# Kernel optimization log

Hardware: AMD Instinct MI355X
Metric: run time of the kernel (lower is better)

Reference implementation:

```python
import jax, jax.numpy as jnp
import numpy as np


def setup_inputs() -> dict:
    key = jax.random.key(0)
    k1, k2, k3, k4 = jax.random.split(key, 4)
    N, E, DI, DO = 8192, 262144, 128, 128
    x = jax.random.normal(k1, (N, DI), dtype=jnp.float32)
    edge_index = jax.random.randint(k2, (2, E), 0, N, dtype=jnp.int64)
    W = jax.random.normal(k3, (DO, DI), dtype=jnp.float32) * (1.0 / np.sqrt(DI))
    b_lin = jax.random.normal(k4, (DO,), dtype=jnp.float32) * 0.01
    bias = jnp.zeros((DO,), dtype=jnp.float32)
    return {"x": x, "edge_index": edge_index, "W": W, "b_lin": b_lin, "bias": bias}


def reference(x, edge_index, W, b_lin, bias):
    # Linear: x @ W^T + b_lin  -> [N, DO]
    h = x @ W.T + b_lin
    N = h.shape[0]
    row, col = edge_index[0], edge_index[1]
    # Dense symmetric adjacency with 1.0 at (row,col) and (col,row); duplicates collapse (set, not add)
    adj = jnp.zeros((N, N), dtype=h.dtype)
    adj = adj.at[row, col].set(1.0)
    adj = adj.at[col, row].set(1.0)
    degree = jnp.sum(adj, axis=1)                      # [N]
    d_inv_sqrt = jnp.power(degree + 1e-6, -0.5)        # [N]
    # D^-1/2 A D^-1/2 as row/col scaling (same math as diag matmuls)
    normalized_adj = d_inv_sqrt[:, None] * adj * d_inv_sqrt[None, :]
    return normalized_adj @ h + bias
```

## Files before the change

kernel.cpp:

```cpp
#include <hip/hip_runtime.h>
#include <hip/hip_bf16.h>


#define DIM 128
#define ROWS_PER_BLOCK 16
#define MAXN 1024

__global__ __launch_bounds__(256) void setup_kernel(
    const float* __restrict__ x, const float* __restrict__ W,
    const float* __restrict__ b, __hip_bfloat16* __restrict__ hb,
    uint4* __restrict__ zero16, int nLin) {
    const int tid = threadIdx.x;
    if ((int)blockIdx.x >= nLin) {
        const long long idx = (long long)((int)blockIdx.x - nLin) * 256 + tid;
        zero16[idx] = make_uint4(0u, 0u, 0u, 0u);
        return;
    }
    __shared__ float xt[ROWS_PER_BLOCK * DIM];
    const int block_row = blockIdx.x * ROWS_PER_BLOCK;
    const float4* xg = reinterpret_cast<const float4*>(x + (long long)block_row * DIM);
    float4* xl = reinterpret_cast<float4*>(xt);
    for (int i = tid; i < ROWS_PER_BLOCK * (DIM / 4); i += 256) xl[i] = xg[i];
    __syncthreads();

    const int d = tid & 127;
    const int half = tid >> 7;
    const float4* W4 = reinterpret_cast<const float4*>(W + (long long)d * DIM);

    float acc[8] = {0.f, 0.f, 0.f, 0.f, 0.f, 0.f, 0.f, 0.f};
    for (int k4 = 0; k4 < DIM / 4; ++k4) {
        const float4 w = W4[k4];
#pragma unroll
        for (int j = 0; j < 8; ++j) {
            const float4 xv =
                reinterpret_cast<const float4*>(xt + (half * 8 + j) * DIM)[k4];
            acc[j] += w.x * xv.x + w.y * xv.y + w.z * xv.z + w.w * xv.w;
        }
    }
    const float bb = b[d];
#pragma unroll
    for (int j = 0; j < 8; ++j) {
        hb[(long long)(block_row + half * 8 + j) * DIM + d] =
            __float2bfloat16(acc[j] + bb);
    }
}

__global__ __launch_bounds__(256) void edge_kernel(
    const int* __restrict__ erow, const int* __restrict__ ecol,
    unsigned int* __restrict__ bitmap, int E, int WPR) {
    const int e = blockIdx.x * 256 + threadIdx.x;
    if (e >= E) return;
    const int r = erow[e];
    const int c = ecol[e];
    atomicOr(bitmap + (long long)r * WPR + (c >> 5), 1u << (c & 31));
    atomicOr(bitmap + (long long)c * WPR + (r >> 5), 1u << (r & 31));
}

__global__ __launch_bounds__(256) void degree_kernel(
    const unsigned int* __restrict__ bitmap, float* __restrict__ dinv, int WPR) {
    const int i = blockIdx.x * 4 + (threadIdx.x >> 6);
    const int lane = threadIdx.x & 63;
    const uint4* rowp = reinterpret_cast<const uint4*>(bitmap + (long long)i * WPR);
    const uint4 v = rowp[lane];
    int cnt = __popc(v.x) + __popc(v.y) + __popc(v.z) + __popc(v.w);
#pragma unroll
    for (int off = 32; off > 0; off >>= 1) cnt += __shfl_down(cnt, off);
    if (lane == 0) dinv[i] = rsqrtf((float)cnt + 1e-6f);
}

__global__ __launch_bounds__(256) void aggregate_kernel(
    const unsigned int* __restrict__ bitmap, const uint4* __restrict__ h16,
    const float* __restrict__ dinv, const float* __restrict__ bias,
    float* __restrict__ out, int WPR) {
    __shared__ int nbr[MAXN];
    __shared__ float wgt[MAXN];
    __shared__ int wave_sums[4];
    __shared__ float partial[16 * DIM];

    const int i = blockIdx.x;
    const int tid = threadIdx.x;
    const float d_i = dinv[i];
    const unsigned int* rowp = bitmap + (long long)i * WPR;

    unsigned int w = (tid < WPR) ? rowp[tid] : 0u;
    const int cnt = __popc(w);

    const int lane = tid & 63;
    const int wave = tid >> 6;
    int scan = cnt;
#pragma unroll
    for (int off = 1; off < 64; off <<= 1) {
        const int v = __shfl_up(scan, off);
        if (lane >= off) scan += v;
    }
    if (lane == 63) wave_sums[wave] = scan;
    __syncthreads();
    int wave_off = 0;
    for (int k = 0; k < wave; ++k) wave_off += wave_sums[k];
    int base = wave_off + scan - cnt;

    while (w) {
        const int bpos = __ffs(w) - 1;
        w &= w - 1;
        const int j = tid * 32 + bpos;
        if (base < MAXN) {
            nbr[base] = j;
            wgt[base] = dinv[j];
        }
        ++base;
    }
    __syncthreads();
    int cnt_total = wave_sums[0] + wave_sums[1] + wave_sums[2] + wave_sums[3];
    if (cnt_total > MAXN) cnt_total = MAXN;

    const int lane16 = tid & 15;
    const int g = tid >> 4;
    float a0 = 0.f, a1 = 0.f, a2 = 0.f, a3 = 0.f;
    float a4 = 0.f, a5 = 0.f, a6 = 0.f, a7 = 0.f;

#define ACC8(v, wv)                                                      \
    {                                                                    \
        a0 += (wv)*__uint_as_float((v).x << 16);                         \
        a1 += (wv)*__uint_as_float((v).x & 0xffff0000u);                 \
        a2 += (wv)*__uint_as_float((v).y << 16);                         \
        a3 += (wv)*__uint_as_float((v).y & 0xffff0000u);                 \
        a4 += (wv)*__uint_as_float((v).z << 16);                         \
        a5 += (wv)*__uint_as_float((v).z & 0xffff0000u);                 \
        a6 += (wv)*__uint_as_float((v).w << 16);                         \
        a7 += (wv)*__uint_as_float((v).w & 0xffff0000u);                 \
    }

    int m = g;
    for (; m + 48 < cnt_total; m += 64) {
        const int j0 = nbr[m], j1 = nbr[m + 16], j2 = nbr[m + 32], j3 = nbr[m + 48];
        const float w0 = wgt[m], w1 = wgt[m + 16], w2 = wgt[m + 32], w3 = wgt[m + 48];
        const uint4 v0 = h16[(j0 << 4) + lane16];
        const uint4 v1 = h16[(j1 << 4) + lane16];
        const uint4 v2 = h16[(j2 << 4) + lane16];
        const uint4 v3 = h16[(j3 << 4) + lane16];
        ACC8(v0, w0);
        ACC8(v1, w1);
        ACC8(v2, w2);
        ACC8(v3, w3);
    }
    for (; m < cnt_total; m += 16) {
        const int j = nbr[m];
        const float wm = wgt[m];
        const uint4 v = h16[(j << 4) + lane16];
        ACC8(v, wm);
    }
#undef ACC8

    float* p = partial + g * DIM + lane16 * 8;
    p[0] = a0; p[1] = a1; p[2] = a2; p[3] = a3;
    p[4] = a4; p[5] = a5; p[6] = a6; p[7] = a7;
    __syncthreads();

    if (tid < DIM) {
        float s = 0.f;
#pragma unroll
        for (int k = 0; k < 16; ++k) s += partial[k * DIM + tid];
        out[(long long)i * DIM + tid] = s * d_i + bias[tid];
    }
}

extern "C" void kernel_launch(void* const* d_in, const int* in_sizes, int n_in,
                              void* d_out, int out_size, void* d_ws, size_t ws_size,
                              hipStream_t stream) {
    const float* x = (const float*)d_in[0];
    const int* ei = (const int*)d_in[1];
    const float* W = (const float*)d_in[2];
    const float* b_lin = (const float*)d_in[3];
    const float* bias = (const float*)d_in[4];
    float* out = (float*)d_out;

    const int N = in_sizes[0] / DIM;
    const int E = in_sizes[1] / 2;
    const int WPR = (N + 31) >> 5;

    unsigned int* bitmap = (unsigned int*)d_ws;
    const long long bitmap_bytes = (long long)N * WPR * 4;
    float* dinv = (float*)((char*)d_ws + bitmap_bytes);
    __hip_bfloat16* hb =
        (__hip_bfloat16*)((char*)d_ws + bitmap_bytes + (long long)N * 4);

    const int nLin = N / ROWS_PER_BLOCK;
    const int nZero = (int)(bitmap_bytes / (256 * 16));
    setup_kernel<<<nLin + nZero, 256, 0, stream>>>(x, W, b_lin, hb,
                                                   (uint4*)bitmap, nLin);
    edge_kernel<<<(E + 255) / 256, 256, 0, stream>>>(ei, ei + E, bitmap, E, WPR);
    degree_kernel<<<N / 4, 256, 0, stream>>>(bitmap, dinv, WPR);
    aggregate_kernel<<<N, 256, 0, stream>>>(bitmap, (const uint4*)hb, dinv, bias,
                                            out, WPR);
}
```

Measured before the change: 63.44 us.

## Prescale features by inverse degree and regroup kernels to overlap edge scatter with linear

Zeroing the bitmap moves to its own kernel with nontemporal stores. The edge atomics and the linear layer now run as one launch on disjoint block ranges, so they can overlap. The degree kernel also multiplies each row of the bf16 h by its own d^-1/2, so the aggregate loop no longer gathers per-neighbor weights or does multiplies. In exchange h is rounded to bf16 a second time after scaling, and the degree kernel does an extra read and write of h.

```diff
diff --git a/kernel.cpp b/kernel.cpp
--- a/kernel.cpp
+++ b/kernel.cpp
@@ -6,18 +6,43 @@
 #define ROWS_PER_BLOCK 16
 #define MAXN 1024
 
-__global__ __launch_bounds__(256) void setup_kernel(
+typedef unsigned int u32x4 __attribute__((ext_vector_type(4)));
+
+__device__ inline unsigned short bf16bits(float f) {
+    __hip_bfloat16 b = __float2bfloat16(f);
+    return *reinterpret_cast<unsigned short*>(&b);
+}
+
+__device__ inline unsigned int scale2(unsigned int p, float s) {
+    const float lo = __uint_as_float(p << 16) * s;
+    const float hi = __uint_as_float(p & 0xffff0000u) * s;
+    return (unsigned int)bf16bits(lo) | ((unsigned int)bf16bits(hi) << 16);
+}
+
+__global__ __launch_bounds__(256) void zero_kernel(u32x4* __restrict__ p) {
+    const int idx = blockIdx.x * 256 + threadIdx.x;
+    u32x4 z = 0;
+    __builtin_nontemporal_store(z, p + idx);
+}
+
+__global__ __launch_bounds__(256) void edge_linear_kernel(
+    const int* __restrict__ erow, const int* __restrict__ ecol,
+    unsigned int* __restrict__ bitmap, int E, int WPR, int nEdge,
     const float* __restrict__ x, const float* __restrict__ W,
-    const float* __restrict__ b, __hip_bfloat16* __restrict__ hb,
-    uint4* __restrict__ zero16, int nLin) {
+    const float* __restrict__ b, __hip_bfloat16* __restrict__ hb) {
     const int tid = threadIdx.x;
-    if ((int)blockIdx.x >= nLin) {
-        const long long idx = (long long)((int)blockIdx.x - nLin) * 256 + tid;
-        zero16[idx] = make_uint4(0u, 0u, 0u, 0u);
+    if ((int)blockIdx.x < nEdge) {
+        const int e = blockIdx.x * 256 + tid;
+        if (e < E) {
+            const int r = erow[e];
+            const int c = ecol[e];
+            atomicOr(bitmap + (long long)r * WPR + (c >> 5), 1u << (c & 31));
+            atomicOr(bitmap + (long long)c * WPR + (r >> 5), 1u << (r & 31));
+        }
         return;
     }
     __shared__ float xt[ROWS_PER_BLOCK * DIM];
-    const int block_row = blockIdx.x * ROWS_PER_BLOCK;
+    const int block_row = ((int)blockIdx.x - nEdge) * ROWS_PER_BLOCK;
     const float4* xg = reinterpret_cast<const float4*>(x + (long long)block_row * DIM);
     float4* xl = reinterpret_cast<float4*>(xt);
     for (int i = tid; i < ROWS_PER_BLOCK * (DIM / 4); i += 256) xl[i] = xg[i];
@@ -45,27 +70,26 @@
     }
 }
 
-__global__ __launch_bounds__(256) void edge_kernel(
-    const int* __restrict__ erow, const int* __restrict__ ecol,
-    unsigned int* __restrict__ bitmap, int E, int WPR) {
-    const int e = blockIdx.x * 256 + threadIdx.x;
-    if (e >= E) return;
-    const int r = erow[e];
-    const int c = ecol[e];
-    atomicOr(bitmap + (long long)r * WPR + (c >> 5), 1u << (c & 31));
-    atomicOr(bitmap + (long long)c * WPR + (r >> 5), 1u << (r & 31));
-}
-
-__global__ __launch_bounds__(256) void degree_kernel(
-    const unsigned int* __restrict__ bitmap, float* __restrict__ dinv, int WPR) {
+__global__ __launch_bounds__(256) void degree_scale_kernel(
+    const unsigned int* __restrict__ bitmap, uint4* __restrict__ h16,
+    float* __restrict__ dinv, int WPR) {
     const int i = blockIdx.x * 4 + (threadIdx.x >> 6);
     const int lane = threadIdx.x & 63;
-    const uint4* rowp = reinterpret_cast<const uint4*>(bitmap + (long long)i * WPR);
-    const uint4 v = rowp[lane];
+    const uint4 v =
+        reinterpret_cast<const uint4*>(bitmap + (long long)i * WPR)[lane];
     int cnt = __popc(v.x) + __popc(v.y) + __popc(v.z) + __popc(v.w);
 #pragma unroll
-    for (int off = 32; off > 0; off >>= 1) cnt += __shfl_down(cnt, off);
-    if (lane == 0) dinv[i] = rsqrtf((float)cnt + 1e-6f);
+    for (int off = 1; off < 64; off <<= 1) cnt += __shfl_xor(cnt, off);
+    const float di = rsqrtf((float)cnt + 1e-6f);
+    if (lane == 0) dinv[i] = di;
+    if (lane < 16) {
+        uint4 hv = h16[i * 16 + lane];
+        hv.x = scale2(hv.x, di);
+        hv.y = scale2(hv.y, di);
+        hv.z = scale2(hv.z, di);
+        hv.w = scale2(hv.w, di);
+        h16[i * 16 + lane] = hv;
+    }
 }
 
 __global__ __launch_bounds__(256) void aggregate_kernel(
@@ -73,7 +97,6 @@
     const float* __restrict__ dinv, const float* __restrict__ bias,
     float* __restrict__ out, int WPR) {
     __shared__ int nbr[MAXN];
-    __shared__ float wgt[MAXN];
     __shared__ int wave_sums[4];
     __shared__ float partial[16 * DIM];
 
@@ -103,10 +126,7 @@
         const int bpos = __ffs(w) - 1;
         w &= w - 1;
         const int j = tid * 32 + bpos;
-        if (base < MAXN) {
-            nbr[base] = j;
-            wgt[base] = dinv[j];
-        }
+        if (base < MAXN) nbr[base] = j;
         ++base;
     }
     __syncthreads();
@@ -118,36 +138,33 @@
     float a0 = 0.f, a1 = 0.f, a2 = 0.f, a3 = 0.f;
     float a4 = 0.f, a5 = 0.f, a6 = 0.f, a7 = 0.f;
 
-#define ACC8(v, wv)                                                      \
-    {                                                                    \
-        a0 += (wv)*__uint_as_float((v).x << 16);                         \
-        a1 += (wv)*__uint_as_float((v).x & 0xffff0000u);                 \
-        a2 += (wv)*__uint_as_float((v).y << 16);                         \
-        a3 += (wv)*__uint_as_float((v).y & 0xffff0000u);                 \
-        a4 += (wv)*__uint_as_float((v).z << 16);                         \
-        a5 += (wv)*__uint_as_float((v).z & 0xffff0000u);                 \
-        a6 += (wv)*__uint_as_float((v).w << 16);                         \
-        a7 += (wv)*__uint_as_float((v).w & 0xffff0000u);                 \
+#define ACC8(v)                                   \
+    {                                             \
+        a0 += __uint_as_float((v).x << 16);       \
+        a1 += __uint_as_float((v).x & 0xffff0000u); \
+        a2 += __uint_as_float((v).y << 16);       \
+        a3 += __uint_as_float((v).y & 0xffff0000u); \
+        a4 += __uint_as_float((v).z << 16);       \
+        a5 += __uint_as_float((v).z & 0xffff0000u); \
+        a6 += __uint_as_float((v).w << 16);       \
+        a7 += __uint_as_float((v).w & 0xffff0000u); \
     }
 
     int m = g;
     for (; m + 48 < cnt_total; m += 64) {
         const int j0 = nbr[m], j1 = nbr[m + 16], j2 = nbr[m + 32], j3 = nbr[m + 48];
-        const float w0 = wgt[m], w1 = wgt[m + 16], w2 = wgt[m + 32], w3 = wgt[m + 48];
         const uint4 v0 = h16[(j0 << 4) + lane16];
         const uint4 v1 = h16[(j1 << 4) + lane16];
         const uint4 v2 = h16[(j2 << 4) + lane16];
         const uint4 v3 = h16[(j3 << 4) + lane16];
-        ACC8(v0, w0);
-        ACC8(v1, w1);
-        ACC8(v2, w2);
-        ACC8(v3, w3);
+        ACC8(v0);
+        ACC8(v1);
+        ACC8(v2);
+        ACC8(v3);
     }
     for (; m < cnt_total; m += 16) {
-        const int j = nbr[m];
-        const float wm = wgt[m];
-        const uint4 v = h16[(j << 4) + lane16];
-        ACC8(v, wm);
+        const uint4 v = h16[(nbr[m] << 4) + lane16];
+        ACC8(v);
     }
 #undef ACC8
 
@@ -184,12 +201,15 @@
     __hip_bfloat16* hb =
         (__hip_bfloat16*)((char*)d_ws + bitmap_bytes + (long long)N * 4);
 
+    const int nZero = (int)(bitmap_bytes / (256 * 16));
+    const int nEdge = (E + 255) / 256;
     const int nLin = N / ROWS_PER_BLOCK;
-    const int nZero = (int)(bitmap_bytes / (256 * 16));
-    setup_kernel<<<nLin + nZero, 256, 0, stream>>>(x, W, b_lin, hb,
-                                                   (uint4*)bitmap, nLin);
-    edge_kernel<<<(E + 255) / 256, 256, 0, stream>>>(ei, ei + E, bitmap, E, WPR);
-    degree_kernel<<<N / 4, 256, 0, stream>>>(bitmap, dinv, WPR);
+
+    zero_kernel<<<nZero, 256, 0, stream>>>((u32x4*)bitmap);
+    edge_linear_kernel<<<nEdge + nLin, 256, 0, stream>>>(ei, ei + E, bitmap, E,
+                                                         WPR, nEdge, x, W, b_lin,
+                                                         hb);
+    degree_scale_kernel<<<N / 4, 256, 0, stream>>>(bitmap, (uint4*)hb, dinv, WPR);
     aggregate_kernel<<<N, 256, 0, stream>>>(bitmap, (const uint4*)hb, dinv, bias,
                                             out, WPR);
 }
```

Result: no change. 64.46 us (median of 2 runs) (+1.6%).
